# Kernel optimization log

Measured on AMD Instinct MI355X. Metric: run time of the kernel, lower is better.

## Reference

```python
import jax, jax.numpy as jnp
import numpy as np

B, NP, NM, C, H = 4, 256, 128, 128, 128
EPS = 1e-5

def layernorm(x, g, b):
    mu = jnp.mean(x, axis=-1, keepdims=True)
    var = jnp.var(x, axis=-1, keepdims=True)
    return (x - mu) * jax.lax.rsqrt(var + EPS) * g + b

def setup_inputs() -> dict:
    key = jax.random.key(0)
    ks = jax.random.split(key, 16)
    s = lambda d: 1.0 / np.sqrt(d)
    return {
        "z": jax.random.normal(ks[0], (B, NP, NM, C), jnp.float32),
        "z_mask": jnp.ones((B, NP, NM), jnp.float32),
        "pocket_pair": jax.random.normal(ks[1], (B, NP, NP, C), jnp.float32),
        "mol_pair": jax.random.normal(ks[2], (B, NM, NM, C), jnp.float32),
        "ln_g": jnp.ones((C,), jnp.float32), "ln_b": jnp.zeros((C,), jnp.float32),
        "lnh_g": jnp.ones((H,), jnp.float32), "lnh_b": jnp.zeros((H,), jnp.float32),
        "gw1": jax.random.uniform(ks[3], (C, H), jnp.float32, -s(C), s(C)),
        "gb1": jnp.zeros((H,), jnp.float32),
        "gw2": jax.random.uniform(ks[4], (C, H), jnp.float32, -s(C), s(C)),
        "gb2": jnp.zeros((H,), jnp.float32),
        "w1": jax.random.uniform(ks[5], (C, H), jnp.float32, -s(C), s(C)),
        "b1": jnp.zeros((H,), jnp.float32),
        "w2": jax.random.uniform(ks[6], (C, H), jnp.float32, -s(C), s(C)),
        "b2": jnp.zeros((H,), jnp.float32),
        "egw": jax.random.uniform(ks[7], (C, C), jnp.float32, -s(C), s(C)),
        "egb": jnp.zeros((C,), jnp.float32),
        "asw": jax.random.uniform(ks[8], (H, C), jnp.float32, -s(H), s(H)),
        "asb": jnp.zeros((C,), jnp.float32),
    }

def reference(z, z_mask, pocket_pair, mol_pair, ln_g, ln_b, lnh_g, lnh_b,
              gw1, gb1, gw2, gb2, w1, b1, w2, b2, egw, egb, asw, asb):
    m = z_mask[..., None]                      # [b,Np,Nm,1]
    zn = layernorm(z, ln_g, ln_b)              # [b,Np,Nm,C]
    pp = layernorm(pocket_pair, ln_g, ln_b)    # [b,Np,Np,C]
    mp = layernorm(mol_pair, ln_g, ln_b)       # [b,Nm,Nm,C]
    gate1 = lambda x: jax.nn.sigmoid(x @ gw1 + gb1) * (x @ w1 + b1)
    gate2 = lambda x: jax.nn.sigmoid(x @ gw2 + gb2) * (x @ w2 + b2)
    ab1 = gate1(zn) * m                        # [b,Np,Nm,H]
    ab2 = gate2(zn) * m                        # [b,Np,Nm,H]
    ppg = gate2(pp)                            # [b,Np,Np,H]
    mpg = gate1(mp)                            # [b,Nm,Nm,H]
    block1 = jnp.einsum('bikc,bkjc->bijc', ppg, ab1)   # [b,Np,Nm,H]
    block2 = jnp.einsum('bikc,bjkc->bijc', ab2, mpg)   # [b,Np,Nm,H]
    h = layernorm(block1 + block2, lnh_g, lnh_b)
    out = jax.nn.sigmoid(zn @ egw + egb) * (h @ asw + asb) * m
    return out
```

## Files before the change

kernel.cpp:

```cpp
#include <hip/hip_runtime.h>
#include <hip/hip_bf16.h>

#define DEVFN __device__ __forceinline__
using bf16 = __hip_bfloat16;
typedef __attribute__((ext_vector_type(8))) short short8;
typedef __attribute__((ext_vector_type(4))) float f32x4;
typedef __attribute__((ext_vector_type(4))) unsigned short us4;

constexpr int BB = 4, NP = 256, NM = 128, CC = 128, HH = 128;
constexpr float EPS = 1e-5f;

#define MFMA16(a,b,c) __builtin_amdgcn_mfma_f32_16x16x32_bf16((a),(b),(c),0,0,0)

DEVFN unsigned short bfbits(float v){ union{ bf16 b; unsigned short s; } u; u.b = __float2bfloat16(v); return u.s; }
DEVFN float bits2f(unsigned short s){ union{ unsigned int i; float f; } u; u.i = ((unsigned)s) << 16; return u.f; }
DEVFN float sigm(float x){ return 1.0f / (1.0f + __expf(-x)); }

__global__ __launch_bounds__(256)
void prep_weights_kernel(const float* __restrict__ gw1, const float* __restrict__ w1,
                         const float* __restrict__ gw2, const float* __restrict__ w2,
                         const float* __restrict__ egw, const float* __restrict__ asw,
                         bf16* __restrict__ wt)
{
  __shared__ float wl[128][129];
  const int bx = blockIdx.x;
  const float* W = (bx==0)?gw1 : (bx==1)?w1 : (bx==2)?gw2 : (bx==3)?w2 : (bx==4)?egw : asw;
  const int t = threadIdx.x;
  for (int i = 0; i < 16; ++i){
    int idx = t + 256*i;
    int k = idx >> 5, n0 = (idx & 31) * 4;
    float4 v = *reinterpret_cast<const float4*>(W + k*128 + n0);
    wl[k][n0] = v.x; wl[k][n0+1] = v.y; wl[k][n0+2] = v.z; wl[k][n0+3] = v.w;
  }
  __syncthreads();
  short* o = reinterpret_cast<short*>(wt) + bx * 16384;
  const int n = t >> 1, kh = t & 1;
  #pragma unroll
  for (int j = 0; j < 8; ++j){
    short8 p;
    #pragma unroll
    for (int u = 0; u < 8; ++u) p[u] = (short)bfbits(wl[kh*64 + j*8 + u][n]);
    *reinterpret_cast<short8*>(o + n*128 + kh*64 + j*8) = p;
  }
}

struct GateSmem {
  short xs[128*128];
  float lgb[2][128];
  float mk[128];
};

DEVFN void gate_pass(const char* xb, const float* mk, int t, long obase, long R,
                     const short* wtg, const short* wtl,
                     const float* __restrict__ bgp, const float* __restrict__ blp,
                     bf16* outp)
{
  const int l = t & 63, w = t >> 6, lr = l & 15, lg = l >> 4;
  const int n0 = w * 32;
  short8 bgf[2][4], blf[2][4];
  #pragma unroll
  for (int nt = 0; nt < 2; ++nt)
    #pragma unroll
    for (int ks = 0; ks < 4; ++ks){
      int n = n0 + nt*16 + lr, ko = ks*32 + lg*8;
      bgf[nt][ks] = *reinterpret_cast<const short8*>(wtg + n*128 + ko);
      blf[nt][ks] = *reinterpret_cast<const short8*>(wtl + n*128 + ko);
    }
  float bgv[2] = { bgp[n0 + lr], bgp[n0 + 16 + lr] };
  float blv[2] = { blp[n0 + lr], blp[n0 + 16 + lr] };
  unsigned short* ob = reinterpret_cast<unsigned short*>(outp);

  for (int mt = 0; mt < 8; ++mt){
    f32x4 zv = {0.f,0.f,0.f,0.f};
    f32x4 ag0 = zv, ag1 = zv, al0 = zv, al1 = zv;
    #pragma unroll
    for (int ks = 0; ks < 4; ++ks){
      int m = mt*16 + lr, ko = ks*32 + lg*8;
      short8 a = *reinterpret_cast<const short8*>(xb + ((m*256 + ko*2) ^ ((m & 7) << 4)));
      ag0 = MFMA16(a, bgf[0][ks], ag0);
      al0 = MFMA16(a, blf[0][ks], al0);
      ag1 = MFMA16(a, bgf[1][ks], ag1);
      al1 = MFMA16(a, blf[1][ks], al1);
    }
    #pragma unroll
    for (int nt = 0; nt < 2; ++nt){
      f32x4 ag = nt ? ag1 : ag0, al = nt ? al1 : al0;
      int h = n0 + nt*16 + lr;
      us4 pk;
      #pragma unroll
      for (int rg = 0; rg < 4; ++rg){
        int rowl = mt*16 + lg*4 + rg;
        float val = sigm(ag[rg] + bgv[nt]) * (al[rg] + blv[nt]) * mk[rowl];
        pk[rg] = bfbits(val);
      }
      *reinterpret_cast<us4*>(ob + obase + (long)h*R + mt*16 + lg*4) = pk;
    }
  }
}

DEVFN void eg_pass(const char* xb, int t, long obase, long R,
                   const short* wtg, const float* __restrict__ bgp, bf16* outp)
{
  const int l = t & 63, w = t >> 6, lr = l & 15, lg = l >> 4;
  const int n0 = w * 32;
  short8 bgf[2][4];
  #pragma unroll
  for (int nt = 0; nt < 2; ++nt)
    #pragma unroll
    for (int ks = 0; ks < 4; ++ks){
      int n = n0 + nt*16 + lr, ko = ks*32 + lg*8;
      bgf[nt][ks] = *reinterpret_cast<const short8*>(wtg + n*128 + ko);
    }
  float bgv[2] = { bgp[n0 + lr], bgp[n0 + 16 + lr] };
  unsigned short* ob = reinterpret_cast<unsigned short*>(outp);

  for (int mt = 0; mt < 8; ++mt){
    f32x4 zv = {0.f,0.f,0.f,0.f};
    f32x4 ag0 = zv, ag1 = zv;
    #pragma unroll
    for (int ks = 0; ks < 4; ++ks){
      int m = mt*16 + lr, ko = ks*32 + lg*8;
      short8 a = *reinterpret_cast<const short8*>(xb + ((m*256 + ko*2) ^ ((m & 7) << 4)));
      ag0 = MFMA16(a, bgf[0][ks], ag0);
      ag1 = MFMA16(a, bgf[1][ks], ag1);
    }
    #pragma unroll
    for (int nt = 0; nt < 2; ++nt){
      f32x4 ag = nt ? ag1 : ag0;
      int h = n0 + nt*16 + lr;
      us4 pk;
      #pragma unroll
      for (int rg = 0; rg < 4; ++rg) pk[rg] = bfbits(sigm(ag[rg] + bgv[nt]));
      *reinterpret_cast<us4*>(ob + obase + (long)h*R + mt*16 + lg*4) = pk;
    }
  }
}

constexpr int NZB = (BB*NP*NM)/128;
constexpr int NPB = (BB*NP*NP)/128;
constexpr int NMB = (BB*NM*NM)/128;

__global__ __launch_bounds__(256, 3)
void gate_all_kernel(const float* __restrict__ z, const float* __restrict__ zmask,
                     const float* __restrict__ pp, const float* __restrict__ mp,
                     const float* __restrict__ lng, const float* __restrict__ lnb,
                     const bf16* __restrict__ wt,
                     const float* __restrict__ gb1, const float* __restrict__ b1,
                     const float* __restrict__ gb2, const float* __restrict__ b2,
                     const float* __restrict__ egbv,
                     bf16* ab1, bf16* ab2, bf16* egp, bf16* ppg, bf16* mpg)
{
  __shared__ GateSmem sm;
  const int t = threadIdx.x;
  const short* wts = reinterpret_cast<const short*>(wt);

  int bx = blockIdx.x;
  const float* x; const float* mask = nullptr;
  long R; int npass = 1;
  const short *w1g, *w1l; const float *bg1v, *bl1v; bf16* o1;
  if (bx < NZB){
    x = z; mask = zmask; R = (long)NP*NM; npass = 3;
    w1g = wts + 0*16384; w1l = wts + 1*16384; bg1v = gb1; bl1v = b1; o1 = ab1;
  } else if (bx < NZB + NPB){
    bx -= NZB; x = pp; R = (long)NP*NP;
    w1g = wts + 2*16384; w1l = wts + 3*16384; bg1v = gb2; bl1v = b2; o1 = ppg;
  } else {
    bx -= NZB + NPB; x = mp; R = (long)NM*NM;
    w1g = wts + 0*16384; w1l = wts + 1*16384; bg1v = gb1; bl1v = b1; o1 = mpg;
  }
  const long row0 = (long)bx * 128;
  const int b = (int)(row0 / R);
  const long rowb = row0 - (long)b * R;
  const long obase = (long)b * 128 * R + rowb;

  if (t < 128){
    sm.lgb[0][t] = lng[t];
    sm.lgb[1][t] = lnb[t];
    sm.mk[t] = mask ? mask[row0 + t] : 1.0f;
  }

  const int r = t >> 1, hf = t & 1;
  const float4* xrow = reinterpret_cast<const float4*>(x + (row0 + r)*128 + hf*64);
  float4 vb[16];
  float s = 0.f, ss = 0.f;
  #pragma unroll
  for (int i = 0; i < 16; ++i){
    float4 v = xrow[i]; vb[i] = v;
    s  += v.x + v.y + v.z + v.w;
    ss += v.x*v.x + v.y*v.y + v.z*v.z + v.w*v.w;
  }
  s  += __shfl_xor(s, 1);
  ss += __shfl_xor(ss, 1);
  const float mu = s * (1.f/128.f);
  const float rsg = rsqrtf(ss * (1.f/128.f) - mu*mu + EPS);
  __syncthreads();
  {
    char* xbw = reinterpret_cast<char*>(sm.xs);
    #pragma unroll
    for (int j = 0; j < 8; ++j){
      float4 a = vb[2*j], c2 = vb[2*j+1];
      float vv[8] = {a.x, a.y, a.z, a.w, c2.x, c2.y, c2.z, c2.w};
      short8 p;
      #pragma unroll
      for (int u = 0; u < 8; ++u){
        int ch = hf*64 + j*8 + u;
        p[u] = (short)bfbits((vv[u] - mu) * rsg * sm.lgb[0][ch] + sm.lgb[1][ch]);
      }
      *reinterpret_cast<short8*>(xbw + ((r*256 + hf*128 + j*16) ^ ((r & 7) << 4))) = p;
    }
  }
  __syncthreads();

  const char* xb = reinterpret_cast<const char*>(sm.xs);
  gate_pass(xb, sm.mk, t, obase, R, w1g, w1l, bg1v, bl1v, o1);
  if (npass == 3){
    gate_pass(xb, sm.mk, t, obase, R, wts + 2*16384, wts + 3*16384, gb2, b2, ab2);
    eg_pass(xb, t, obase, R, wts + 4*16384, egbv, egp);
  }
}

DEVFN int b1swz(int j){ return (((j & 7) ^ ((j >> 3) & 7)) << 4); }

__global__ __launch_bounds__(256, 2)
void einsum_mfma_kernel(const bf16* __restrict__ ppg, const bf16* __restrict__ ab1,
                        const bf16* __restrict__ ab2, const bf16* __restrict__ mpg,
                        bf16* __restrict__ bsum)
{
  __shared__ short b1t[128*256];
  const int t = threadIdx.x, l = t & 63, w = t >> 6, lr = l & 15, lg = l >> 4;
  const int bc = blockIdx.x;
  const short* A1 = reinterpret_cast<const short*>(ppg) + (long)bc * (NP*NP);
  const short* B1 = reinterpret_cast<const short*>(ab1) + (long)bc * (NP*NM);
  const short* A2 = reinterpret_cast<const short*>(ab2) + (long)bc * (NP*NM);
  const short* B2 = reinterpret_cast<const short*>(mpg) + (long)bc * (NM*NM);

  char* lb = reinterpret_cast<char*>(b1t);
  for (int it = 0; it < 16; ++it){
    int idx = t + 256*it;
    int k = idx >> 4, j0 = (idx & 15) * 8;
    short8 v = *reinterpret_cast<const short8*>(B1 + idx*8);
    #pragma unroll
    for (int u = 0; u < 8; ++u){
      int j = j0 + u;
      *reinterpret_cast<short*>(lb + ((j*512 + k*2) ^ b1swz(j))) = v[u];
    }
  }
  __syncthreads();

  f32x4 zv = {0.f,0.f,0.f,0.f};
  f32x4 acc[4][8];
  #pragma unroll
  for (int i = 0; i < 4; ++i)
    #pragma unroll
    for (int j = 0; j < 8; ++j) acc[i][j] = zv;

  const int m0 = w * 64;
  for (int ks = 0; ks < 8; ++ks){
    int ko = ks*32 + lg*8;
    short8 af[4];
    #pragma unroll
    for (int mt = 0; mt < 4; ++mt)
      af[mt] = *reinterpret_cast<const short8*>(A1 + (m0 + mt*16 + lr)*256 + ko);
    short8 bf[8];
    #pragma unroll
    for (int nt = 0; nt < 8; ++nt){
      int n = nt*16 + lr;
      bf[nt] = *reinterpret_cast<const short8*>(lb + ((n*512 + ko*2) ^ b1swz(n)));
    }
    #pragma unroll
    for (int mt = 0; mt < 4; ++mt)
      #pragma unroll
      for (int nt = 0; nt < 8; ++nt)
        acc[mt][nt] = MFMA16(af[mt], bf[nt], acc[mt][nt]);
  }
  for (int ks = 0; ks < 4; ++ks){
    int ko = ks*32 + lg*8;
    short8 af[4];
    #pragma unroll
    for (int mt = 0; mt < 4; ++mt)
      af[mt] = *reinterpret_cast<const short8*>(A2 + (m0 + mt*16 + lr)*128 + ko);
    short8 bf[8];
    #pragma unroll
    for (int nt = 0; nt < 8; ++nt)
      bf[nt] = *reinterpret_cast<const short8*>(B2 + (nt*16 + lr)*128 + ko);
    #pragma unroll
    for (int mt = 0; mt < 4; ++mt)
      #pragma unroll
      for (int nt = 0; nt < 8; ++nt)
        acc[mt][nt] = MFMA16(af[mt], bf[nt], acc[mt][nt]);
  }
  unsigned short* out = reinterpret_cast<unsigned short*>(bsum) + (long)bc * (NP*NM);
  #pragma unroll
  for (int mt = 0; mt < 4; ++mt)
    #pragma unroll
    for (int nt = 0; nt < 8; ++nt)
      #pragma unroll
      for (int rg = 0; rg < 4; ++rg)
        out[(m0 + mt*16 + lg*4 + rg)*128 + nt*16 + lr] = bfbits(acc[mt][nt][rg]);
}

__global__ __launch_bounds__(256, 2)
void final_mfma_kernel(const bf16* __restrict__ bsum, const bf16* __restrict__ eg,
                       const float* __restrict__ mask,
                       const float* __restrict__ lnhg, const float* __restrict__ lnhb,
                       const bf16* __restrict__ wt, const float* __restrict__ asb,
                       float* __restrict__ out)
{
  __shared__ struct {
    short xsT[128][72];
    short xs[64*128];
    float lgb[2][128];
    float ps[4][64], pss[4][64];
    float mu[64], rs[64], mk[64];
  } sm;
  const int t = threadIdx.x, l = t & 63, w = t >> 6, lr = l & 15, lg = l >> 4;
  const long row0 = (long)blockIdx.x * 64;
  const int b = (int)(row0 >> 15);
  const long rowb = row0 & 32767;

  if (t < 128){ sm.lgb[0][t] = lnhg[t]; sm.lgb[1][t] = lnhb[t]; }
  if (t < 64) sm.mk[t] = mask[row0 + t];

  const short* bs = reinterpret_cast<const short*>(bsum);
  #pragma unroll
  for (int i = 0; i < 4; ++i){
    int idx = t + 256*i;
    int c = idx >> 3, j8 = idx & 7;
    short8 v = *reinterpret_cast<const short8*>(bs + (long)(b*128 + c)*32768 + rowb + j8*8);
    *reinterpret_cast<short8*>(&sm.xsT[c][j8*8]) = v;
  }
  __syncthreads();
  {
    int ij = t & 63, q = t >> 6;
    float s = 0.f, ss = 0.f;
    #pragma unroll
    for (int k = 0; k < 32; ++k){
      float v = bits2f((unsigned short)sm.xsT[q*32 + k][ij]);
      s += v; ss += v*v;
    }
    sm.ps[q][ij] = s; sm.pss[q][ij] = ss;
  }
  __syncthreads();
  if (t < 64){
    float s  = sm.ps[0][t] + sm.ps[1][t] + sm.ps[2][t] + sm.ps[3][t];
    float ss = sm.pss[0][t] + sm.pss[1][t] + sm.pss[2][t] + sm.pss[3][t];
    float mu = s * (1.f/128.f);
    float var = ss * (1.f/128.f) - mu*mu;
    sm.mu[t] = mu; sm.rs[t] = rsqrtf(var + EPS);
  }
  __syncthreads();
  {
    int ij = t & 63, q = t >> 6;
    float mu = sm.mu[ij], rg2 = sm.rs[ij];
    char* xbw = reinterpret_cast<char*>(sm.xs);
    #pragma unroll
    for (int u = 0; u < 4; ++u){
      short8 p;
      #pragma unroll
      for (int e = 0; e < 8; ++e){
        int c = q*32 + u*8 + e;
        float v = bits2f((unsigned short)sm.xsT[c][ij]);
        p[e] = (short)bfbits((v - mu) * rg2 * sm.lgb[0][c] + sm.lgb[1][c]);
      }
      *reinterpret_cast<short8*>(xbw + ((ij*256 + q*64 + u*16) ^ ((ij & 7) << 4))) = p;
    }
  }
  __syncthreads();

  const short* aswt = reinterpret_cast<const short*>(wt) + 5*16384;
  f32x4 zv = {0.f,0.f,0.f,0.f};
  f32x4 acc[8];
  #pragma unroll
  for (int i = 0; i < 8; ++i) acc[i] = zv;
  const char* xb = reinterpret_cast<const char*>(sm.xs);
  #pragma unroll
  for (int ks = 0; ks < 4; ++ks){
    int m = w*16 + lr, ko = ks*32 + lg*8;
    short8 a = *reinterpret_cast<const short8*>(xb + ((m*256 + ko*2) ^ ((m & 7) << 4)));
    #pragma unroll
    for (int nt = 0; nt < 8; ++nt){
      short8 bfr = *reinterpret_cast<const short8*>(aswt + (nt*16 + lr)*128 + ko);
      acc[nt] = MFMA16(a, bfr, acc[nt]);
    }
  }
  const unsigned short* egb2 = reinterpret_cast<const unsigned short*>(eg);
  #pragma unroll
  for (int nt = 0; nt < 8; ++nt){
    int co = nt*16 + lr;
    float bias = asb[co];
    us4 egv = *reinterpret_cast<const us4*>(egb2 + (long)(b*128 + co)*32768 + rowb + w*16 + lg*4);
    #pragma unroll
    for (int rg = 0; rg < 4; ++rg){
      int rowl = w*16 + lg*4 + rg;
      float val = bits2f(egv[rg]) * (acc[nt][rg] + bias) * sm.mk[rowl];
      out[(row0 + rowl)*128 + co] = val;
    }
  }
}

extern "C" void kernel_launch(void* const* d_in, const int* in_sizes, int n_in,
                              void* d_out, int out_size, void* d_ws, size_t ws_size,
                              hipStream_t stream)
{
  const float* z     = (const float*)d_in[0];
  const float* zmask = (const float*)d_in[1];
  const float* pp    = (const float*)d_in[2];
  const float* mp    = (const float*)d_in[3];
  const float* ln_g  = (const float*)d_in[4];
  const float* ln_b  = (const float*)d_in[5];
  const float* lnh_g = (const float*)d_in[6];
  const float* lnh_b = (const float*)d_in[7];
  const float* gw1   = (const float*)d_in[8];
  const float* gb1   = (const float*)d_in[9];
  const float* gw2   = (const float*)d_in[10];
  const float* gb2   = (const float*)d_in[11];
  const float* w1    = (const float*)d_in[12];
  const float* b1    = (const float*)d_in[13];
  const float* w2    = (const float*)d_in[14];
  const float* b2    = (const float*)d_in[15];
  const float* egw   = (const float*)d_in[16];
  const float* egb   = (const float*)d_in[17];
  const float* asw   = (const float*)d_in[18];
  const float* asb   = (const float*)d_in[19];
  float* out = (float*)d_out;

  const size_t ZE = (size_t)BB*NP*NM*HH;
  const size_t PE = (size_t)BB*NP*NP*HH;
  const size_t ME = (size_t)BB*NM*NM*HH;
  char* ws = (char*)d_ws;
  size_t off = 0;
  bf16* wt   = (bf16*)(ws + off); off += 6 * 16384 * 2;
  bf16* ab1  = (bf16*)(ws + off); off += ZE * 2;
  bf16* ab2  = (bf16*)(ws + off); off += ZE * 2;
  bf16* egp  = (bf16*)(ws + off); off += ZE * 2;
  bf16* ppg  = (bf16*)(ws + off); off += PE * 2;
  bf16* mpg  = (bf16*)(ws + off); off += ME * 2;
  bf16* bsum = (bf16*)(ws + off); off += ZE * 2;
  if (ws_size < off) return;

  prep_weights_kernel<<<6, 256, 0, stream>>>(gw1, w1, gw2, w2, egw, asw, wt);

  gate_all_kernel<<<NZB + NPB + NMB, 256, 0, stream>>>(
      z, zmask, pp, mp, ln_g, ln_b, wt,
      gb1, b1, gb2, b2, egb,
      ab1, ab2, egp, ppg, mpg);

  einsum_mfma_kernel<<<BB*CC, 256, 0, stream>>>(ppg, ab1, ab2, mpg, bsum);

  final_mfma_kernel<<<(BB*NP*NM)/64, 256, 0, stream>>>(
      bsum, egp, zmask, lnh_g, lnh_b, wt, asb, out);
}
```

Measured before the change: 250.5 us.

## Store gated intermediates in row-block-tiled layout for contiguous channel writes

Changes the layout of the gated intermediates (ab1, ab2, ppg, mpg, eg). They were channel-major planes of length R. They are now blocked so that each 128-row block stores a contiguous 128x128 tile indexed [channel][row-in-block]. Gate-pass writes then land in one contiguous 32KB region per block instead of 128 strided planes. The einsum and final kernels recompute their addresses to read the tiled layout, so einsum A/B loads become strided across 16384-element tiles, which may hurt their locality.

Measured after the change: 245.7 us, median of 2. Within noise of the previous version (-1.9%).

```diff
diff --git a/kernel.cpp b/kernel.cpp
--- a/kernel.cpp
+++ b/kernel.cpp
@@ -15,6 +15,7 @@
 DEVFN unsigned short bfbits(float v){ union{ bf16 b; unsigned short s; } u; u.b = __float2bfloat16(v); return u.s; }
 DEVFN float bits2f(unsigned short s){ union{ unsigned int i; float f; } u; u.i = ((unsigned)s) << 16; return u.f; }
 DEVFN float sigm(float x){ return 1.0f / (1.0f + __expf(-x)); }
+
 
 __global__ __launch_bounds__(256)
 void prep_weights_kernel(const float* __restrict__ gw1, const float* __restrict__ w1,
@@ -50,7 +51,7 @@
   float mk[128];
 };
 
-DEVFN void gate_pass(const char* xb, const float* mk, int t, long obase, long R,
+DEVFN void gate_pass(const char* xb, const float* mk, int t, long obase,
                      const short* wtg, const short* wtl,
                      const float* __restrict__ bgp, const float* __restrict__ blp,
                      bf16* outp)
@@ -93,12 +94,12 @@
         float val = sigm(ag[rg] + bgv[nt]) * (al[rg] + blv[nt]) * mk[rowl];
         pk[rg] = bfbits(val);
       }
-      *reinterpret_cast<us4*>(ob + obase + (long)h*R + mt*16 + lg*4) = pk;
-    }
-  }
-}
-
-DEVFN void eg_pass(const char* xb, int t, long obase, long R,
+      *reinterpret_cast<us4*>(ob + obase + h*128 + mt*16 + lg*4) = pk;
+    }
+  }
+}
+
+DEVFN void eg_pass(const char* xb, int t, long obase,
                    const short* wtg, const float* __restrict__ bgp, bf16* outp)
 {
   const int l = t & 63, w = t >> 6, lr = l & 15, lg = l >> 4;
@@ -131,7 +132,7 @@
       us4 pk;
       #pragma unroll
       for (int rg = 0; rg < 4; ++rg) pk[rg] = bfbits(sigm(ag[rg] + bgv[nt]));
-      *reinterpret_cast<us4*>(ob + obase + (long)h*R + mt*16 + lg*4) = pk;
+      *reinterpret_cast<us4*>(ob + obase + h*128 + mt*16 + lg*4) = pk;
     }
   }
 }
@@ -171,7 +172,7 @@
   const long row0 = (long)bx * 128;
   const int b = (int)(row0 / R);
   const long rowb = row0 - (long)b * R;
-  const long obase = (long)b * 128 * R + rowb;
+  const long obase = ((long)b * (R >> 7) + (rowb >> 7)) * 16384;
 
   if (t < 128){
     sm.lgb[0][t] = lng[t];
@@ -212,10 +213,10 @@
   __syncthreads();
 
   const char* xb = reinterpret_cast<const char*>(sm.xs);
-  gate_pass(xb, sm.mk, t, obase, R, w1g, w1l, bg1v, bl1v, o1);
+  gate_pass(xb, sm.mk, t, obase, w1g, w1l, bg1v, bl1v, o1);
   if (npass == 3){
-    gate_pass(xb, sm.mk, t, obase, R, wts + 2*16384, wts + 3*16384, gb2, b2, ab2);
-    eg_pass(xb, t, obase, R, wts + 4*16384, egbv, egp);
+    gate_pass(xb, sm.mk, t, obase, wts + 2*16384, wts + 3*16384, gb2, b2, ab2);
+    eg_pass(xb, t, obase, wts + 4*16384, egbv, egp);
   }
 }
 
@@ -229,16 +230,21 @@
   __shared__ short b1t[128*256];
   const int t = threadIdx.x, l = t & 63, w = t >> 6, lr = l & 15, lg = l >> 4;
   const int bc = blockIdx.x;
-  const short* A1 = reinterpret_cast<const short*>(ppg) + (long)bc * (NP*NP);
-  const short* B1 = reinterpret_cast<const short*>(ab1) + (long)bc * (NP*NM);
-  const short* A2 = reinterpret_cast<const short*>(ab2) + (long)bc * (NP*NM);
-  const short* B2 = reinterpret_cast<const short*>(mpg) + (long)bc * (NM*NM);
+  const int b = bc >> 7, c = bc & 127;
+  const short* A1s = reinterpret_cast<const short*>(ppg);
+  const short* B1s = reinterpret_cast<const short*>(ab1);
+  const short* A2s = reinterpret_cast<const short*>(ab2);
+  const short* B2s = reinterpret_cast<const short*>(mpg);
+  const long a1base = ((long)b*512*128 + c) * 128;
+  const long b1base = ((long)b*256*128 + c) * 128;
+  const long a2base = ((long)b*256*128 + c) * 128;
+  const long b2base = ((long)b*128*128 + c) * 128;
 
   char* lb = reinterpret_cast<char*>(b1t);
   for (int it = 0; it < 16; ++it){
     int idx = t + 256*it;
     int k = idx >> 4, j0 = (idx & 15) * 8;
-    short8 v = *reinterpret_cast<const short8*>(B1 + idx*8);
+    short8 v = *reinterpret_cast<const short8*>(B1s + b1base + (long)k*16384 + j0);
     #pragma unroll
     for (int u = 0; u < 8; ++u){
       int j = j0 + u;
@@ -257,10 +263,13 @@
   const int m0 = w * 64;
   for (int ks = 0; ks < 8; ++ks){
     int ko = ks*32 + lg*8;
+    int koh = ko >> 7, kol = ko & 127;
     short8 af[4];
     #pragma unroll
-    for (int mt = 0; mt < 4; ++mt)
-      af[mt] = *reinterpret_cast<const short8*>(A1 + (m0 + mt*16 + lr)*256 + ko);
+    for (int mt = 0; mt < 4; ++mt){
+      long m = m0 + mt*16 + lr;
+      af[mt] = *reinterpret_cast<const short8*>(A1s + a1base + m*32768 + (long)koh*16384 + kol);
+    }
     short8 bf[8];
     #pragma unroll
     for (int nt = 0; nt < 8; ++nt){
@@ -277,12 +286,16 @@
     int ko = ks*32 + lg*8;
     short8 af[4];
     #pragma unroll
-    for (int mt = 0; mt < 4; ++mt)
-      af[mt] = *reinterpret_cast<const short8*>(A2 + (m0 + mt*16 + lr)*128 + ko);
+    for (int mt = 0; mt < 4; ++mt){
+      long m = m0 + mt*16 + lr;
+      af[mt] = *reinterpret_cast<const short8*>(A2s + a2base + m*16384 + ko);
+    }
     short8 bf[8];
     #pragma unroll
-    for (int nt = 0; nt < 8; ++nt)
-      bf[nt] = *reinterpret_cast<const short8*>(B2 + (nt*16 + lr)*128 + ko);
+    for (int nt = 0; nt < 8; ++nt){
+      long n = nt*16 + lr;
+      bf[nt] = *reinterpret_cast<const short8*>(B2s + b2base + n*16384 + ko);
+    }
     #pragma unroll
     for (int mt = 0; mt < 4; ++mt)
       #pragma unroll
@@ -384,11 +397,13 @@
     }
   }
   const unsigned short* egb2 = reinterpret_cast<const unsigned short*>(eg);
+  const long egbase = ((long)b*256 + (rowb >> 7)) * 16384;
+  const int rsub = (int)(rowb & 64);
   #pragma unroll
   for (int nt = 0; nt < 8; ++nt){
     int co = nt*16 + lr;
     float bias = asb[co];
-    us4 egv = *reinterpret_cast<const us4*>(egb2 + (long)(b*128 + co)*32768 + rowb + w*16 + lg*4);
+    us4 egv = *reinterpret_cast<const us4*>(egb2 + egbase + co*128 + rsub + w*16 + lg*4);
     #pragma unroll
     for (int rg = 0; rg < 4; ++rg){
       int rowl = w*16 + lg*4 + rg;
```
